# Kernel tuning notes

Hardware: AMD Instinct MI355X
Metric: run time of the kernel (lower is better)

The kernel has to match this reference:

```python
import jax, jax.numpy as jnp
import numpy as np

NEG_SLOPE = 0.2  # PyG GATv2Conv default leaky_relu slope
N_NODES = 50000
N_EDGES = 800000
F_IN = 128
HID = 32
HEADS = 4
OUT_HEADS = 1
N_CLS = 16
MLP_HID = 128


def topk_mask(score, dst, k, num_nodes):
    """Boolean mask [E,H]: True where edge score is among top-k for its destination."""
    E = score.shape[0]
    counts = jnp.zeros((num_nodes,), jnp.int32).at[dst].add(1)
    starts = jnp.cumsum(counts) - counts  # first sorted index of each dst segment

    def one_head(s):
        o1 = jnp.argsort(-s)                       # sort by score desc
        o2 = jnp.argsort(dst[o1], stable=True)     # stable sort by dst -> (dst asc, score desc)
        perm = o1[o2]
        rank = jnp.arange(E) - starts[dst[perm]]   # rank within dst segment
        return jnp.zeros((E,), bool).at[perm].set(rank < k)

    return jax.vmap(one_head, in_axes=1, out_axes=1)(score)


def masked_segment_softmax(score, mask, dst, num_nodes):
    neg = jnp.where(mask, score, -jnp.inf)
    m = jax.ops.segment_max(neg, dst, num_segments=num_nodes)
    m = jnp.where(jnp.isfinite(m), m, 0.0)
    ex = jnp.where(mask, jnp.exp(score - m[dst]), 0.0)
    s = jax.ops.segment_sum(ex, dst, num_segments=num_nodes)
    return ex / (s[dst] + 1e-16)


def gatv2_topk(x, edge_index, k, Wl, Wr, att, b, heads, out_c, concat, num_nodes):
    src, dst = edge_index[0], edge_index[1]
    xl = (x @ Wl).reshape(num_nodes, heads, out_c)
    xr = (x @ Wr).reshape(num_nodes, heads, out_c)
    h = xl[src] + xr[dst]                                   # [E,H,C]
    e = jnp.einsum('ehc,hc->eh', jax.nn.leaky_relu(h, NEG_SLOPE), att)  # [E,H]
    keep = topk_mask(e, dst, k, num_nodes)
    alpha = masked_segment_softmax(e, keep, dst, num_nodes)       # top-k attention
    alpha_n = masked_segment_softmax(e, ~keep, dst, num_nodes)    # truncated (noise) attention
    msg = xl[src]                                                  # [E,H,C]
    out = jax.ops.segment_sum(alpha[..., None] * msg, dst, num_segments=num_nodes)
    noise = jax.ops.segment_sum(alpha_n[..., None] * msg, dst, num_segments=num_nodes)
    if concat:
        out = out.reshape(num_nodes, heads * out_c)
        noise = noise.reshape(num_nodes, heads * out_c)
    else:
        out = out.mean(axis=1)
        noise = noise.mean(axis=1)
    return out + b, noise + b


def setup_inputs() -> dict:
    key = jax.random.key(0)
    ks = jax.random.split(key, 14)
    s = 0.1
    x = jax.random.normal(ks[0], (N_NODES, F_IN), jnp.float32)
    edge_index = jax.random.randint(ks[1], (2, N_EDGES), 0, N_NODES, dtype=jnp.int64)
    return {
        'x': x,
        'edge_index': edge_index,
        'attn_topk': 8,
        'Wl1': jax.random.normal(ks[2], (F_IN, HEADS * HID), jnp.float32) * s,
        'Wr1': jax.random.normal(ks[3], (F_IN, HEADS * HID), jnp.float32) * s,
        'att1': jax.random.normal(ks[4], (HEADS, HID), jnp.float32) * s,
        'b1': jnp.zeros((HEADS * HID,), jnp.float32),
        'Wl2': jax.random.normal(ks[5], (HEADS * HID, OUT_HEADS * N_CLS), jnp.float32) * s,
        'Wr2': jax.random.normal(ks[6], (HEADS * HID, OUT_HEADS * N_CLS), jnp.float32) * s,
        'att2': jax.random.normal(ks[7], (OUT_HEADS, N_CLS), jnp.float32) * s,
        'b2': jnp.zeros((N_CLS,), jnp.float32),
        'lin1_w': jax.random.normal(ks[8], (HEADS * HID, MLP_HID), jnp.float32) * s,
        'lin1_b': jnp.zeros((MLP_HID,), jnp.float32),
        'lin2_w': jax.random.normal(ks[9], (MLP_HID, N_CLS), jnp.float32) * s,
        'lin2_b': jnp.zeros((N_CLS,), jnp.float32),
    }


def reference(x, edge_index, attn_topk, Wl1, Wr1, att1, b1, Wl2, Wr2, att2, b2,
              lin1_w, lin1_b, lin2_w, lin2_b):
    # eval mode: dropout is identity
    h, noise1 = gatv2_topk(x, edge_index, attn_topk, Wl1, Wr1, att1, b1,
                           HEADS, HID, True, N_NODES)
    h = jax.nn.elu(h)
    n1 = jax.nn.elu(noise1 @ lin1_w + lin1_b) @ lin2_w + lin2_b
    out, noise2 = gatv2_topk(h, edge_index, attn_topk, Wl2, Wr2, att2, b2,
                             OUT_HEADS, N_CLS, False, N_NODES)
    return (jax.nn.log_softmax(out, axis=1),
            jax.nn.log_softmax(n1, axis=1),
            jax.nn.log_softmax(noise2, axis=1))
```

## Files before the change

kernel.cpp:

```cpp
#include <hip/hip_runtime.h>
#include <math.h>

#define NN 50000
#define NE 800000
#define FIN 128
#define HEADS 4
#define HID 32
#define D1 128
#define NCLS 16
#define NEG 0.2f
#define NINF (-3.402823466e38f)
#define CAP 64
#define SB 256
#define NSB ((NN + SB - 1) / SB)

typedef unsigned long long ull;

__global__ void k_count(const int* __restrict__ dst, int* __restrict__ counts) {
  int j = blockIdx.x * 256 + threadIdx.x;
  if (j < NE) atomicAdd(&counts[dst[j]], 1);
}

__global__ void k_scanA(const int* __restrict__ counts, int* __restrict__ bsum) {
  int b = blockIdx.x, t = threadIdx.x;
  int idx = b * SB + t;
  int v = idx < NN ? counts[idx] : 0;
  __shared__ int ws[4];
#pragma unroll
  for (int o = 1; o <= 32; o <<= 1) v += __shfl_xor(v, o, 64);
  if ((t & 63) == 0) ws[t >> 6] = v;
  __syncthreads();
  if (t == 0) bsum[b] = ws[0] + ws[1] + ws[2] + ws[3];
}

__global__ void k_scanB(const int* __restrict__ bsum, int* __restrict__ boff) {
  int t = threadIdx.x;
  int v = t < NSB ? bsum[t] : 0;
  __shared__ int tmp[256];
  tmp[t] = v;
  __syncthreads();
  for (int o = 1; o < 256; o <<= 1) {
    int u = t >= o ? tmp[t - o] : 0;
    __syncthreads();
    tmp[t] += u;
    __syncthreads();
  }
  if (t < NSB) boff[t] = tmp[t] - v;
}

__global__ void k_scanC(const int* __restrict__ counts, const int* __restrict__ boff,
                        int* __restrict__ starts, int* __restrict__ cursor) {
  int b = blockIdx.x, t = threadIdx.x;
  int idx = b * SB + t;
  int v = idx < NN ? counts[idx] : 0;
  __shared__ int tmp[256];
  tmp[t] = v;
  __syncthreads();
  for (int o = 1; o < 256; o <<= 1) {
    int u = t >= o ? tmp[t - o] : 0;
    __syncthreads();
    tmp[t] += u;
    __syncthreads();
  }
  int ex = tmp[t] - v + boff[b];
  if (idx < NN) { starts[idx] = ex; cursor[idx] = ex; }
}

__global__ void k_scatter(const int* __restrict__ src, const int* __restrict__ dst,
                          int* __restrict__ cursor, int* __restrict__ eperm,
                          int* __restrict__ sperm) {
  int j = blockIdx.x * 256 + threadIdx.x;
  if (j < NE) {
    int p = atomicAdd(&cursor[dst[j]], 1);
    eperm[p] = j;
    sperm[p] = src[j];
  }
}

template <int BM, int BN, int BK, int TM, int TN, int ACT>
__global__ __launch_bounds__(256) void k_gemm2(
    const float* __restrict__ A, const float* __restrict__ B1,
    const float* __restrict__ B2, int N1, int s1, int s2,
    const float* __restrict__ bias, float* __restrict__ C, int M, int N, int K) {
  constexpr int NT = (BM / TM) * (BN / TN);
  static_assert(NT == 256, "block must be 256 threads");
  static_assert(TM % 4 == 0 && TN % 4 == 0, "float4 fragments");
  __shared__ float As[BK][BM + 4];
  __shared__ float Bs[BK][BN];
  int tid = threadIdx.x;
  int bm = blockIdx.y * BM, bn = blockIdx.x * BN;
  constexpr int TX = BN / TN;
  int tn = (tid % TX) * TN;
  int tm = (tid / TX) * TM;
  float acc[TM][TN];
#pragma unroll
  for (int i = 0; i < TM; i++)
#pragma unroll
    for (int j = 0; j < TN; j++) acc[i][j] = 0.f;

  for (int k0 = 0; k0 < K; k0 += BK) {
    constexpr int AV = BM * BK / 4;
    for (int i = tid; i < AV; i += NT) {
      int r = i / (BK / 4);
      int c4 = (i % (BK / 4)) * 4;
      float4 v = make_float4(0.f, 0.f, 0.f, 0.f);
      int gr = bm + r;
      if (gr < M) v = *(const float4*)(A + (size_t)gr * K + k0 + c4);
      As[c4 + 0][r] = v.x; As[c4 + 1][r] = v.y; As[c4 + 2][r] = v.z; As[c4 + 3][r] = v.w;
    }
    constexpr int BV = BK * BN / 4;
    for (int i = tid; i < BV; i += NT) {
      int r = i / (BN / 4), c4 = (i % (BN / 4)) * 4;
      int gc = bn + c4, gk = k0 + r;
      float4 v = (gc < N1) ? *(const float4*)(B1 + (size_t)gk * s1 + gc)
                           : *(const float4*)(B2 + (size_t)gk * s2 + (gc - N1));
      Bs[r][c4 + 0] = v.x; Bs[r][c4 + 1] = v.y; Bs[r][c4 + 2] = v.z; Bs[r][c4 + 3] = v.w;
    }
    __syncthreads();
#pragma unroll
    for (int kk = 0; kk < BK; kk++) {
      float ra[TM], rb[TN];
#pragma unroll
      for (int i = 0; i < TM; i += 4)
        *(float4*)&ra[i] = *(const float4*)&As[kk][tm + i];
#pragma unroll
      for (int j = 0; j < TN; j += 4)
        *(float4*)&rb[j] = *(const float4*)&Bs[kk][tn + j];
#pragma unroll
      for (int i = 0; i < TM; i++)
#pragma unroll
        for (int j = 0; j < TN; j++) acc[i][j] += ra[i] * rb[j];
    }
    __syncthreads();
  }
#pragma unroll
  for (int i = 0; i < TM; i++) {
    int gr = bm + tm + i;
    if (gr >= M) continue;
#pragma unroll
    for (int j = 0; j < TN; j += 4) {
      float4 v;
      v.x = acc[i][j + 0]; v.y = acc[i][j + 1]; v.z = acc[i][j + 2]; v.w = acc[i][j + 3];
      if (bias) {
        v.x += bias[bn + tn + j + 0]; v.y += bias[bn + tn + j + 1];
        v.z += bias[bn + tn + j + 2]; v.w += bias[bn + tn + j + 3];
      }
      if (ACT == 1) {
        v.x = v.x > 0.f ? v.x : expm1f(v.x);
        v.y = v.y > 0.f ? v.y : expm1f(v.y);
        v.z = v.z > 0.f ? v.z : expm1f(v.z);
        v.w = v.w > 0.f ? v.w : expm1f(v.w);
      }
      *(float4*)(C + (size_t)gr * N + bn + tn + j) = v;
    }
  }
}

__device__ __forceinline__ unsigned fkey(float f) {
  unsigned u = __float_as_uint(f);
  return u ^ (((int)u >> 31) | 0x80000000u);
}

__global__ __launch_bounds__(256) void k_fused1(
    const float* __restrict__ xlr, const float* __restrict__ att,
    const int* __restrict__ sperm, const int* __restrict__ eperm,
    const int* __restrict__ starts, const int* __restrict__ counts,
    const int* __restrict__ kptr, const float* __restrict__ bias,
    float* __restrict__ hout, float* __restrict__ nout) {
  __shared__ float sc[4][CAP][4];
  __shared__ ull keys[4][4][CAP + 1];
  int w = threadIdx.x >> 6;
  int l = threadIdx.x & 63;
  int d = blockIdx.x * 4 + w;
  if (d >= NN) return;
  int st = starts[d];
  int deg = counts[d];
  if (deg > CAP) deg = CAP;
  int k = kptr[0];

  int srcreg = 0, idreg = 0x7fffffff;
  if (l < deg) { srcreg = sperm[st + l]; idreg = eperm[st + l]; }

  int h2 = l >> 5, li = l & 31;
  int headq = li >> 3;
  float4 xrv = *(const float4*)(xlr + (size_t)d * 256 + 128 + 4 * li);
  float4 attv = *(const float4*)(att + 4 * li);
  float4 b1v = *(const float4*)(bias + 4 * li);

  float4 xc[8];
#pragma unroll
  for (int j = 0; j < 8; j++) xc[j] = make_float4(0.f, 0.f, 0.f, 0.f);

#pragma unroll
  for (int Q = 0; Q < 16; Q += 8) {
    if (Q < deg) {
      int rr[4]; float4 xv[4]; float pp[4]; bool vv[4];
#pragma unroll
      for (int j = 0; j < 4; j++) {
        rr[j] = Q + 2 * j + h2;
        int s = __shfl(srcreg, rr[j]);
        vv[j] = rr[j] < deg;
        xv[j] = make_float4(0.f, 0.f, 0.f, 0.f);
        if (vv[j]) xv[j] = *(const float4*)(xlr + (size_t)s * 256 + 4 * li);
        xc[Q / 2 + j] = xv[j];
      }
#pragma unroll
      for (int j = 0; j < 4; j++) {
        float a, p = 0.f;
        a = xv[j].x + xrv.x; p += fmaxf(a, NEG * a) * attv.x;
        a = xv[j].y + xrv.y; p += fmaxf(a, NEG * a) * attv.y;
        a = xv[j].z + xrv.z; p += fmaxf(a, NEG * a) * attv.z;
        a = xv[j].w + xrv.w; p += fmaxf(a, NEG * a) * attv.w;
        pp[j] = p;
      }
#pragma unroll
      for (int o = 1; o <= 4; o <<= 1) {
#pragma unroll
        for (int j = 0; j < 4; j++) pp[j] += __shfl_xor(pp[j], o, 64);
      }
      if ((li & 7) == 0) {
#pragma unroll
        for (int j = 0; j < 4; j++)
          if (vv[j]) sc[w][rr[j]][headq] = pp[j];
      }
    }
  }
  for (int q = 16; q < deg; q += 8) {
    int rr[4]; float4 xv[4]; float pp[4]; bool vv[4];
#pragma unroll
    for (int j = 0; j < 4; j++) {
      rr[j] = q + 2 * j + h2;
      int s = __shfl(srcreg, rr[j]);
      vv[j] = rr[j] < deg;
      xv[j] = make_float4(0.f, 0.f, 0.f, 0.f);
      if (vv[j]) xv[j] = *(const float4*)(xlr + (size_t)s * 256 + 4 * li);
    }
#pragma unroll
    for (int j = 0; j < 4; j++) {
      float a, p = 0.f;
      a = xv[j].x + xrv.x; p += fmaxf(a, NEG * a) * attv.x;
      a = xv[j].y + xrv.y; p += fmaxf(a, NEG * a) * attv.y;
      a = xv[j].z + xrv.z; p += fmaxf(a, NEG * a) * attv.z;
      a = xv[j].w + xrv.w; p += fmaxf(a, NEG * a) * attv.w;
      pp[j] = p;
    }
#pragma unroll
    for (int o = 1; o <= 4; o <<= 1) {
#pragma unroll
      for (int j = 0; j < 4; j++) pp[j] += __shfl_xor(pp[j], o, 64);
    }
    if ((li & 7) == 0) {
#pragma unroll
      for (int j = 0; j < 4; j++)
        if (vv[j]) sc[w][rr[j]][headq] = pp[j];
    }
  }

  int hh = l >> 4, ii = l & 15;
  float sv[4]; bool val[4]; ull mkey[4]; int rank[4];
#pragma unroll
  for (int j = 0; j < 4; j++) {
    int q = j * 16 + ii;
    val[j] = q < deg;
    sv[j] = val[j] ? sc[w][q][hh] : NINF;
    int bid = __shfl(idreg, q);
    mkey[j] = val[j] ? (((ull)fkey(sv[j]) << 32) | (unsigned)~bid) : 0ull;
    rank[j] = 0;
    if (val[j]) keys[w][hh][q] = mkey[j];
  }
  int nch = (deg + 15) >> 4;
  const ull* kp = keys[w][hh];
  if (nch == 1) {
    int r0 = 0;
    for (int p = 0; p < deg; p++) r0 += kp[p] > mkey[0];
    rank[0] = r0;
  } else if (nch == 2) {
    int r0 = 0, r1 = 0;
    for (int p = 0; p < deg; p++) {
      ull bk = kp[p];
      r0 += bk > mkey[0]; r1 += bk > mkey[1];
    }
    rank[0] = r0; rank[1] = r1;
  } else {
    for (int p = 0; p < deg; p++) {
      ull bk = kp[p];
#pragma unroll
      for (int j = 0; j < 4; j++) rank[j] += bk > mkey[j];
    }
  }
  bool kept[4];
#pragma unroll
  for (int j = 0; j < 4; j++) kept[j] = val[j] && (rank[j] < k);

  float mk = fmaxf(fmaxf(sv[0], sv[1]), fmaxf(sv[2], sv[3]));
  float mn = NINF;
#pragma unroll
  for (int j = 0; j < 4; j++) mn = fmaxf(mn, kept[j] ? NINF : sv[j]);
#pragma unroll
  for (int o = 1; o <= 8; o <<= 1) {
    mk = fmaxf(mk, __shfl_xor(mk, o, 64));
    mn = fmaxf(mn, __shfl_xor(mn, o, 64));
  }
  float ek[4], en[4], sk = 0.f, sn = 0.f;
#pragma unroll
  for (int j = 0; j < 4; j++) {
    ek[j] = kept[j] ? __expf(sv[j] - mk) : 0.f;
    en[j] = (val[j] && !kept[j]) ? __expf(sv[j] - mn) : 0.f;
    sk += ek[j]; sn += en[j];
  }
#pragma unroll
  for (int o = 1; o <= 8; o <<= 1) {
    sk += __shfl_xor(sk, o, 64);
    sn += __shfl_xor(sn, o, 64);
  }
  float ik = 1.f / (sk + 1e-16f), inn = 1.f / (sn + 1e-16f);
#pragma unroll
  for (int j = 0; j < 4; j++) {
    if (val[j]) sc[w][j * 16 + ii][hh] = kept[j] ? ek[j] * ik : -(en[j] * inn);
  }

  float4 ao = make_float4(0.f, 0.f, 0.f, 0.f), an = ao;
#pragma unroll
  for (int j = 0; j < 8; j++) {
    int r = 2 * j + h2;
    if (r < deg) {
      float wv = sc[w][r][headq];
      float pw = fmaxf(wv, 0.f), nw = pw - wv;
      float4 xv = xc[j];
      ao.x += pw * xv.x; ao.y += pw * xv.y; ao.z += pw * xv.z; ao.w += pw * xv.w;
      an.x += nw * xv.x; an.y += nw * xv.y; an.z += nw * xv.z; an.w += nw * xv.w;
    }
  }
  for (int q = 16; q < deg; q += 4) {
    int r0 = q + h2, r1 = q + 2 + h2;
    int s0 = __shfl(srcreg, r0), s1 = __shfl(srcreg, r1);
    if (r0 < deg) {
      float wv = sc[w][r0][headq];
      float pw = fmaxf(wv, 0.f), nw = pw - wv;
      float4 xv = *(const float4*)(xlr + (size_t)s0 * 256 + 4 * li);
      ao.x += pw * xv.x; ao.y += pw * xv.y; ao.z += pw * xv.z; ao.w += pw * xv.w;
      an.x += nw * xv.x; an.y += nw * xv.y; an.z += nw * xv.z; an.w += nw * xv.w;
    }
    if (r1 < deg) {
      float wv = sc[w][r1][headq];
      float pw = fmaxf(wv, 0.f), nw = pw - wv;
      float4 xv = *(const float4*)(xlr + (size_t)s1 * 256 + 4 * li);
      ao.x += pw * xv.x; ao.y += pw * xv.y; ao.z += pw * xv.z; ao.w += pw * xv.w;
      an.x += nw * xv.x; an.y += nw * xv.y; an.z += nw * xv.z; an.w += nw * xv.w;
    }
  }
  ao.x += __shfl_xor(ao.x, 32, 64); ao.y += __shfl_xor(ao.y, 32, 64);
  ao.z += __shfl_xor(ao.z, 32, 64); ao.w += __shfl_xor(ao.w, 32, 64);
  an.x += __shfl_xor(an.x, 32, 64); an.y += __shfl_xor(an.y, 32, 64);
  an.z += __shfl_xor(an.z, 32, 64); an.w += __shfl_xor(an.w, 32, 64);
  if (h2 == 0) {
    float4 vo;
    vo.x = ao.x + b1v.x; vo.y = ao.y + b1v.y; vo.z = ao.z + b1v.z; vo.w = ao.w + b1v.w;
    vo.x = vo.x > 0.f ? vo.x : expm1f(vo.x);
    vo.y = vo.y > 0.f ? vo.y : expm1f(vo.y);
    vo.z = vo.z > 0.f ? vo.z : expm1f(vo.z);
    vo.w = vo.w > 0.f ? vo.w : expm1f(vo.w);
    *(float4*)(hout + (size_t)d * D1 + 4 * li) = vo;
  } else {
    float4 vn;
    vn.x = an.x + b1v.x; vn.y = an.y + b1v.y; vn.z = an.z + b1v.z; vn.w = an.w + b1v.w;
    *(float4*)(nout + (size_t)d * D1 + 4 * li) = vn;
  }
}

__global__ __launch_bounds__(256) void k_fused2(
    const float* __restrict__ xlr, const float* __restrict__ att,
    const int* __restrict__ sperm, const int* __restrict__ eperm,
    const int* __restrict__ starts, const int* __restrict__ counts,
    const int* __restrict__ kptr, const float* __restrict__ bias,
    float* __restrict__ out0, float* __restrict__ out1) {
  __shared__ float sc[4][CAP];
  __shared__ ull keys[4][CAP];
  int w = threadIdx.x >> 6;
  int l = threadIdx.x & 63;
  int d = blockIdx.x * 4 + w;
  if (d >= NN) return;
  int st = starts[d];
  int deg = counts[d];
  if (deg > CAP) deg = CAP;
  int k = kptr[0];

  int srcreg = 0, idreg = 0x7fffffff;
  if (l < deg) { srcreg = sperm[st + l]; idreg = eperm[st + l]; }

  int g = l >> 4, li = l & 15;
  float xrv = xlr[(size_t)d * 32 + 16 + li];
  float attv = att[li];
  float bv2 = bias[li];

  float xc[8];
#pragma unroll
  for (int j = 0; j < 8; j++) xc[j] = 0.f;

#pragma unroll
  for (int Q = 0; Q < 32; Q += 8) {
    if (Q < deg) {
      int r0 = Q + g, r1 = Q + 4 + g;
      int s0 = __shfl(srcreg, r0), s1 = __shfl(srcreg, r1);
      float x0 = (r0 < deg) ? xlr[(size_t)s0 * 32 + li] : 0.f;
      float x1 = (r1 < deg) ? xlr[(size_t)s1 * 32 + li] : 0.f;
      xc[Q / 4] = x0; xc[Q / 4 + 1] = x1;
      float a0 = x0 + xrv, a1 = x1 + xrv;
      float p0 = fmaxf(a0, NEG * a0) * attv;
      float p1 = fmaxf(a1, NEG * a1) * attv;
#pragma unroll
      for (int o = 1; o <= 8; o <<= 1) {
        p0 += __shfl_xor(p0, o, 64);
        p1 += __shfl_xor(p1, o, 64);
      }
      if (li == 0) {
        if (r0 < deg) sc[w][r0] = p0;
        if (r1 < deg) sc[w][r1] = p1;
      }
    }
  }
  for (int q = 32; q < deg; q += 8) {
    int r0 = q + g, r1 = q + 4 + g;
    int s0 = __shfl(srcreg, r0), s1 = __shfl(srcreg, r1);
    float x0 = (r0 < deg) ? xlr[(size_t)s0 * 32 + li] : 0.f;
    float x1 = (r1 < deg) ? xlr[(size_t)s1 * 32 + li] : 0.f;
    float a0 = x0 + xrv, a1 = x1 + xrv;
    float p0 = fmaxf(a0, NEG * a0) * attv;
    float p1 = fmaxf(a1, NEG * a1) * attv;
#pragma unroll
    for (int o = 1; o <= 8; o <<= 1) {
      p0 += __shfl_xor(p0, o, 64);
      p1 += __shfl_xor(p1, o, 64);
    }
    if (li == 0) {
      if (r0 < deg) sc[w][r0] = p0;
      if (r1 < deg) sc[w][r1] = p1;
    }
  }

  float sv = (l < deg) ? sc[w][l] : NINF;
  ull mk64 = (l < deg) ? (((ull)fkey(sv) << 32) | (unsigned)~idreg) : 0ull;
  if (l < deg) keys[w][l] = mk64;
  int rank = 0;
  for (int p = 0; p < deg; p++) rank += keys[w][p] > mk64;
  bool kept = (l < deg) && (rank < k);

  float mk = sv, mn = kept ? NINF : sv;
#pragma unroll
  for (int o = 1; o <= 32; o <<= 1) {
    mk = fmaxf(mk, __shfl_xor(mk, o, 64));
    mn = fmaxf(mn, __shfl_xor(mn, o, 64));
  }
  float ek = kept ? __expf(sv - mk) : 0.f;
  float en = ((l < deg) && !kept) ? __expf(sv - mn) : 0.f;
  float sk = ek, sn = en;
#pragma unroll
  for (int o = 1; o <= 32; o <<= 1) {
    sk += __shfl_xor(sk, o, 64);
    sn += __shfl_xor(sn, o, 64);
  }
  if (l < deg) sc[w][l] = kept ? ek / (sk + 1e-16f) : -(en / (sn + 1e-16f));

  float ao = 0.f, an = 0.f;
#pragma unroll
  for (int j = 0; j < 8; j++) {
    int r = 4 * j + g;
    if (r < deg) {
      float wv = sc[w][r];
      float pw = fmaxf(wv, 0.f), nw = pw - wv;
      ao += pw * xc[j]; an += nw * xc[j];
    }
  }
  for (int q = 32; q < deg; q += 4) {
    int r = q + g;
    int s = __shfl(srcreg, r);
    if (r < deg) {
      float wv = sc[w][r];
      float pw = fmaxf(wv, 0.f), nw = pw - wv;
      float xv = xlr[(size_t)s * 32 + li];
      ao += pw * xv; an += nw * xv;
    }
  }
  ao += __shfl_xor(ao, 16, 64); ao += __shfl_xor(ao, 32, 64);
  an += __shfl_xor(an, 16, 64); an += __shfl_xor(an, 32, 64);
  float vo = ao + bv2, vn = an + bv2;
  float mo = vo, mv = vn;
#pragma unroll
  for (int o = 1; o <= 8; o <<= 1) {
    mo = fmaxf(mo, __shfl_xor(mo, o, 64));
    mv = fmaxf(mv, __shfl_xor(mv, o, 64));
  }
  float eo = __expf(vo - mo), ev = __expf(vn - mv);
#pragma unroll
  for (int o = 1; o <= 8; o <<= 1) {
    eo += __shfl_xor(eo, o, 64);
    ev += __shfl_xor(ev, o, 64);
  }
  if (g == 0) out0[(size_t)d * NCLS + li] = vo - (mo + logf(eo));
  if (g == 1) out1[(size_t)d * NCLS + li] = vn - (mv + logf(ev));
}

__global__ void k_lsm(const float* __restrict__ in, float* __restrict__ out) {
  int r = blockIdx.x * 256 + threadIdx.x;
  if (r >= NN) return;
  const float4* p = (const float4*)(in + (size_t)r * NCLS);
  float4 a = p[0], b = p[1], c = p[2], d4 = p[3];
  float vals[16] = {a.x, a.y, a.z, a.w, b.x, b.y, b.z, b.w,
                    c.x, c.y, c.z, c.w, d4.x, d4.y, d4.z, d4.w};
  float m = vals[0];
#pragma unroll
  for (int i = 1; i < 16; i++) m = fmaxf(m, vals[i]);
  float s = 0.f;
#pragma unroll
  for (int i = 0; i < 16; i++) s += expf(vals[i] - m);
  float l = m + logf(s);
  float* op = out + (size_t)r * NCLS;
#pragma unroll
  for (int i = 0; i < 16; i++) op[i] = vals[i] - l;
}

extern "C" void kernel_launch(void* const* d_in, const int* in_sizes, int n_in,
                              void* d_out, int out_size, void* d_ws, size_t ws_size,
                              hipStream_t stream) {
  (void)in_sizes; (void)n_in; (void)out_size; (void)ws_size;
  const float* x    = (const float*)d_in[0];
  const int*   ei   = (const int*)d_in[1];
  const int*   kptr = (const int*)d_in[2];
  const float* Wl1  = (const float*)d_in[3];
  const float* Wr1  = (const float*)d_in[4];
  const float* att1 = (const float*)d_in[5];
  const float* b1   = (const float*)d_in[6];
  const float* Wl2  = (const float*)d_in[7];
  const float* Wr2  = (const float*)d_in[8];
  const float* att2 = (const float*)d_in[9];
  const float* b2   = (const float*)d_in[10];
  const float* l1w  = (const float*)d_in[11];
  const float* l1b  = (const float*)d_in[12];
  const float* l2w  = (const float*)d_in[13];
  const float* l2b  = (const float*)d_in[14];
  const int* srcv = ei;
  const int* dstv = ei + NE;

  char* wp = (char*)d_ws;
  auto alloc = [&](size_t n) { char* p = wp; wp += (n + 255) & ~(size_t)255; return p; };
  float* xlr1   = (float*)alloc((size_t)NN * 256 * 4);
  float* hbuf   = (float*)alloc((size_t)NN * D1 * 4);
  float* noise1 = (float*)alloc((size_t)NN * D1 * 4);
  float* t1     = (float*)alloc((size_t)NN * D1 * 4);
  float* xlr2   = (float*)alloc((size_t)NN * 32 * 4);
  float* n1buf  = (float*)alloc((size_t)NN * NCLS * 4);
  int* counts = (int*)alloc((size_t)NN * 4);
  int* starts = (int*)alloc((size_t)NN * 4);
  int* cursor = (int*)alloc((size_t)NN * 4);
  int* eperm  = (int*)alloc((size_t)NE * 4);
  int* sperm  = (int*)alloc((size_t)NE * 4);
  int* bsum   = (int*)alloc((size_t)NSB * 4);
  int* boff   = (int*)alloc((size_t)NSB * 4);

  hipMemsetAsync(counts, 0, (size_t)NN * 4, stream);
  k_count<<<(NE + 255) / 256, 256, 0, stream>>>(dstv, counts);
  k_scanA<<<NSB, 256, 0, stream>>>(counts, bsum);
  k_scanB<<<1, 256, 0, stream>>>(bsum, boff);
  k_scanC<<<NSB, 256, 0, stream>>>(counts, boff, starts, cursor);
  k_scatter<<<(NE + 255) / 256, 256, 0, stream>>>(srcv, dstv, cursor, eperm, sperm);

  k_gemm2<64, 128, 32, 4, 8, 0><<<dim3(2, (NN + 63) / 64), 256, 0, stream>>>(
      x, Wl1, Wr1, 128, 128, 128, nullptr, xlr1, NN, 256, FIN);

  k_fused1<<<(NN + 3) / 4, 256, 0, stream>>>(xlr1, att1, sperm, eperm,
                                             starts, counts, kptr, b1, hbuf, noise1);

  k_gemm2<64, 128, 32, 4, 8, 1><<<dim3(1, (NN + 63) / 64), 256, 0, stream>>>(
      noise1, l1w, l1w, 128, 128, 128, l1b, t1, NN, 128, 128);
  k_gemm2<256, 16, 32, 4, 4, 0><<<dim3(1, (NN + 255) / 256), 256, 0, stream>>>(
      t1, l2w, l2w, 16, 16, 16, l2b, n1buf, NN, NCLS, 128);

  k_gemm2<128, 32, 32, 4, 4, 0><<<dim3(1, (NN + 127) / 128), 256, 0, stream>>>(
      hbuf, Wl2, Wr2, 16, 16, 16, nullptr, xlr2, NN, 32, D1);

  float* o = (float*)d_out;
  k_fused2<<<(NN + 3) / 4, 256, 0, stream>>>(xlr2, att2, sperm, eperm, starts,
                                             counts, kptr, b2, o,
                                             o + (size_t)2 * NN * NCLS);

  k_lsm<<<(NN + 255) / 256, 256, 0, stream>>>(n1buf, o + (size_t)NN * NCLS);
}
```

Before: 455.8 us.

## Run noise MLP branch in bf16 with MFMA and fuse log-softmax

The noise1 output of the first fused kernel is now stored as bf16. The two-layer noise MLP is rewritten as MFMA 16x16x32 bf16 kernels using pre-transposed bf16 weights, with the intermediate activation kept in bf16. The final log-softmax is folded into the second MLP kernel, which removes the separate k_lsm pass and the n1buf round trip. This cuts memory traffic and replaces the fp32 SIMT GEMMs with matrix-core work, at the cost of bf16 rounding in that output branch and an extra small weight-conversion launch.

```diff
diff --git a/kernel.cpp b/kernel.cpp
--- a/kernel.cpp
+++ b/kernel.cpp
@@ -15,6 +15,14 @@
 #define NSB ((NN + SB - 1) / SB)
 
 typedef unsigned long long ull;
+typedef __attribute__((ext_vector_type(8))) short bf16x8;
+typedef __attribute__((ext_vector_type(4))) float f32x4;
+
+__device__ __forceinline__ short f2bf(float v) {
+  unsigned u = __float_as_uint(v);
+  unsigned r = (u + 0x7fffu + ((u >> 16) & 1u)) >> 16;
+  return (short)r;
+}
 
 __global__ void k_count(const int* __restrict__ dst, int* __restrict__ counts) {
   int j = blockIdx.x * 256 + threadIdx.x;
@@ -156,6 +164,86 @@
   }
 }
 
+__global__ void k_cvtw(const float* __restrict__ l1w, const float* __restrict__ l2w,
+                       short* __restrict__ w1t, short* __restrict__ w2t) {
+  int t = blockIdx.x * 256 + threadIdx.x;
+  if (t < 128 * 128) {
+    int n = t >> 7, k = t & 127;
+    w1t[t] = f2bf(l1w[k * 128 + n]);
+  }
+  if (t < 16 * 128) {
+    int n = t >> 7, k = t & 127;
+    w2t[t] = f2bf(l2w[k * 16 + n]);
+  }
+}
+
+__global__ __launch_bounds__(256) void k_mlp1(
+    const short* __restrict__ A, const short* __restrict__ BT,
+    const float* __restrict__ bias, short* __restrict__ C) {
+  int wv = threadIdx.x >> 6, lane = threadIdx.x & 63;
+  int m0 = (blockIdx.x * 4 + wv) * 16;
+  int quad = lane >> 4;
+  int mr = m0 + (lane & 15);
+  bool mok = mr < NN;
+  bf16x8 afr[4];
+#pragma unroll
+  for (int kt = 0; kt < 4; kt++) {
+    bf16x8 z = {0, 0, 0, 0, 0, 0, 0, 0};
+    afr[kt] = mok ? *(const bf16x8*)(A + (size_t)mr * 128 + kt * 32 + quad * 8) : z;
+  }
+#pragma unroll
+  for (int nt = 0; nt < 8; nt++) {
+    f32x4 acc = {0.f, 0.f, 0.f, 0.f};
+    int nc = nt * 16 + (lane & 15);
+#pragma unroll
+    for (int kt = 0; kt < 4; kt++) {
+      bf16x8 bfr = *(const bf16x8*)(BT + (size_t)nc * 128 + kt * 32 + quad * 8);
+      acc = __builtin_amdgcn_mfma_f32_16x16x32_bf16(afr[kt], bfr, acc, 0, 0, 0);
+    }
+    float bval = bias[nc];
+#pragma unroll
+    for (int r = 0; r < 4; r++) {
+      int row = m0 + quad * 4 + r;
+      if (row < NN) {
+        float v = acc[r] + bval;
+        v = v > 0.f ? v : expm1f(v);
+        C[(size_t)row * 128 + nc] = f2bf(v);
+      }
+    }
+  }
+}
+
+__global__ __launch_bounds__(256) void k_mlp2(
+    const short* __restrict__ A, const short* __restrict__ BT,
+    const float* __restrict__ bias, float* __restrict__ out) {
+  int wv = threadIdx.x >> 6, lane = threadIdx.x & 63;
+  int m0 = (blockIdx.x * 4 + wv) * 16;
+  int quad = lane >> 4, col = lane & 15;
+  int mr = m0 + col;
+  bool mok = mr < NN;
+  f32x4 acc = {0.f, 0.f, 0.f, 0.f};
+#pragma unroll
+  for (int kt = 0; kt < 4; kt++) {
+    bf16x8 z = {0, 0, 0, 0, 0, 0, 0, 0};
+    bf16x8 afr = mok ? *(const bf16x8*)(A + (size_t)mr * 128 + kt * 32 + quad * 8) : z;
+    bf16x8 bfr = *(const bf16x8*)(BT + (size_t)col * 128 + kt * 32 + quad * 8);
+    acc = __builtin_amdgcn_mfma_f32_16x16x32_bf16(afr, bfr, acc, 0, 0, 0);
+  }
+  float bval = bias[col];
+#pragma unroll
+  for (int r = 0; r < 4; r++) {
+    float v = acc[r] + bval;
+    float m = v;
+#pragma unroll
+    for (int o = 1; o <= 8; o <<= 1) m = fmaxf(m, __shfl_xor(m, o, 64));
+    float e = __expf(v - m), s = e;
+#pragma unroll
+    for (int o = 1; o <= 8; o <<= 1) s += __shfl_xor(s, o, 64);
+    int row = m0 + quad * 4 + r;
+    if (row < NN) out[(size_t)row * NCLS + col] = v - (m + logf(s));
+  }
+}
+
 __device__ __forceinline__ unsigned fkey(float f) {
   unsigned u = __float_as_uint(f);
   return u ^ (((int)u >> 31) | 0x80000000u);
@@ -166,7 +254,7 @@
     const int* __restrict__ sperm, const int* __restrict__ eperm,
     const int* __restrict__ starts, const int* __restrict__ counts,
     const int* __restrict__ kptr, const float* __restrict__ bias,
-    float* __restrict__ hout, float* __restrict__ nout) {
+    float* __restrict__ hout, short* __restrict__ nout) {
   __shared__ float sc[4][CAP][4];
   __shared__ ull keys[4][4][CAP + 1];
   int w = threadIdx.x >> 6;
@@ -362,9 +450,10 @@
     vo.w = vo.w > 0.f ? vo.w : expm1f(vo.w);
     *(float4*)(hout + (size_t)d * D1 + 4 * li) = vo;
   } else {
-    float4 vn;
-    vn.x = an.x + b1v.x; vn.y = an.y + b1v.y; vn.z = an.z + b1v.z; vn.w = an.w + b1v.w;
-    *(float4*)(nout + (size_t)d * D1 + 4 * li) = vn;
+    short4 vn;
+    vn.x = f2bf(an.x + b1v.x); vn.y = f2bf(an.y + b1v.y);
+    vn.z = f2bf(an.z + b1v.z); vn.w = f2bf(an.w + b1v.w);
+    *(short4*)(nout + (size_t)d * D1 + 4 * li) = vn;
   }
 }
 
@@ -498,25 +587,6 @@
   }
   if (g == 0) out0[(size_t)d * NCLS + li] = vo - (mo + logf(eo));
   if (g == 1) out1[(size_t)d * NCLS + li] = vn - (mv + logf(ev));
-}
-
-__global__ void k_lsm(const float* __restrict__ in, float* __restrict__ out) {
-  int r = blockIdx.x * 256 + threadIdx.x;
-  if (r >= NN) return;
-  const float4* p = (const float4*)(in + (size_t)r * NCLS);
-  float4 a = p[0], b = p[1], c = p[2], d4 = p[3];
-  float vals[16] = {a.x, a.y, a.z, a.w, b.x, b.y, b.z, b.w,
-                    c.x, c.y, c.z, c.w, d4.x, d4.y, d4.z, d4.w};
-  float m = vals[0];
-#pragma unroll
-  for (int i = 1; i < 16; i++) m = fmaxf(m, vals[i]);
-  float s = 0.f;
-#pragma unroll
-  for (int i = 0; i < 16; i++) s += expf(vals[i] - m);
-  float l = m + logf(s);
-  float* op = out + (size_t)r * NCLS;
-#pragma unroll
-  for (int i = 0; i < 16; i++) op[i] = vals[i] - l;
 }
 
 extern "C" void kernel_launch(void* const* d_in, const int* in_sizes, int n_in,
@@ -545,10 +615,11 @@
   auto alloc = [&](size_t n) { char* p = wp; wp += (n + 255) & ~(size_t)255; return p; };
   float* xlr1   = (float*)alloc((size_t)NN * 256 * 4);
   float* hbuf   = (float*)alloc((size_t)NN * D1 * 4);
-  float* noise1 = (float*)alloc((size_t)NN * D1 * 4);
-  float* t1     = (float*)alloc((size_t)NN * D1 * 4);
+  short* noise1 = (short*)alloc((size_t)NN * D1 * 2);
+  short* t1     = (short*)alloc((size_t)NN * D1 * 2);
   float* xlr2   = (float*)alloc((size_t)NN * 32 * 4);
-  float* n1buf  = (float*)alloc((size_t)NN * NCLS * 4);
+  short* w1t    = (short*)alloc((size_t)128 * 128 * 2);
+  short* w2t    = (short*)alloc((size_t)16 * 128 * 2);
   int* counts = (int*)alloc((size_t)NN * 4);
   int* starts = (int*)alloc((size_t)NN * 4);
   int* cursor = (int*)alloc((size_t)NN * 4);
@@ -564,24 +635,23 @@
   k_scanC<<<NSB, 256, 0, stream>>>(counts, boff, starts, cursor);
   k_scatter<<<(NE + 255) / 256, 256, 0, stream>>>(srcv, dstv, cursor, eperm, sperm);
 
+  k_cvtw<<<64, 256, 0, stream>>>(l1w, l2w, w1t, w2t);
+
   k_gemm2<64, 128, 32, 4, 8, 0><<<dim3(2, (NN + 63) / 64), 256, 0, stream>>>(
       x, Wl1, Wr1, 128, 128, 128, nullptr, xlr1, NN, 256, FIN);
 
   k_fused1<<<(NN + 3) / 4, 256, 0, stream>>>(xlr1, att1, sperm, eperm,
                                              starts, counts, kptr, b1, hbuf, noise1);
 
-  k_gemm2<64, 128, 32, 4, 8, 1><<<dim3(1, (NN + 63) / 64), 256, 0, stream>>>(
-      noise1, l1w, l1w, 128, 128, 128, l1b, t1, NN, 128, 128);
-  k_gemm2<256, 16, 32, 4, 4, 0><<<dim3(1, (NN + 255) / 256), 256, 0, stream>>>(
-      t1, l2w, l2w, 16, 16, 16, l2b, n1buf, NN, NCLS, 128);
+  float* o = (float*)d_out;
+
+  k_mlp1<<<(NN + 63) / 64, 256, 0, stream>>>(noise1, w1t, l1b, t1);
+  k_mlp2<<<(NN + 63) / 64, 256, 0, stream>>>(t1, w2t, l2b, o + (size_t)NN * NCLS);
 
   k_gemm2<128, 32, 32, 4, 4, 0><<<dim3(1, (NN + 127) / 128), 256, 0, stream>>>(
       hbuf, Wl2, Wr2, 16, 16, 16, nullptr, xlr2, NN, 32, D1);
 
-  float* o = (float*)d_out;
   k_fused2<<<(NN + 3) / 4, 256, 0, stream>>>(xlr2, att2, sperm, eperm, starts,
                                              counts, kptr, b2, o,
                                              o + (size_t)2 * NN * NCLS);
-
-  k_lsm<<<(NN + 255) / 256, 256, 0, stream>>>(n1buf, o + (size_t)NN * NCLS);
-}
+}
```

New measurement: 424.6 us (median of 2 runs). 1.07x faster.
